# Performance work log

Measured on AMD Instinct MI355X. Metric: run time of the kernel, lower is better.

Reference implementation:

```python
import jax, jax.numpy as jnp
import numpy as np

B, C, P, N_PARTS, JOINTS_PER_PART = 2048, 256, 15, 5, 3
GROUPS = 4
EPS = 1e-5
MASK_VAL = 10000.0


def setup_inputs() -> dict:
    key = jax.random.key(0)
    k1, k2, k3 = jax.random.split(key, 3)
    g = (2 * C) // GROUPS  # 128
    return {
        "x": jax.random.normal(k1, (B, C, P, 1), jnp.float32),
        "conv_w": jax.random.normal(k2, (GROUPS, g, g), jnp.float32) * 0.05,
        "conv_b": jax.random.normal(k3, (2 * C,), jnp.float32) * 0.05,
        "bn_gamma": jnp.ones((2 * C,), jnp.float32),
        "bn_beta": jnp.zeros((2 * C,), jnp.float32),
    }


def reference(x, conv_w, conv_b, bn_gamma, bn_beta):
    Bb, Cc, Pp, _ = x.shape
    xs = x[..., 0]  # [B, C, P]

    # relative[b,c,i,k] = xs[b,c,k] - xs[b,c,i]; for a row i in part p the
    # reduction is max_k(relative - MASK_VAL * [k in part p]). Since the mask
    # only depends on the part of row i, precompute the per-part masked max of
    # xs over k and broadcast-subtract xs[i].
    part_id = jnp.arange(Pp) // JOINTS_PER_PART  # [P]
    Mg = jnp.where(part_id[None, :] == jnp.arange(N_PARTS)[:, None], -MASK_VAL, 0.0)  # [5, P]
    m = jnp.max(xs[:, :, None, :] + Mg[None, None, :, :], axis=-1)  # [B, C, 5]
    tmp = m[:, :, part_id] - xs  # [B, C, P]

    y = jnp.concatenate([xs, tmp], axis=1)  # [B, 2C, P]

    # grouped 1x1 conv (groups=4)
    g = (2 * Cc) // GROUPS
    y4 = y.reshape(Bb, GROUPS, g, Pp)
    z = jnp.einsum('bgip,goi->bgop', y4, conv_w).reshape(Bb, 2 * Cc, Pp)
    z = z + conv_b[None, :, None]

    # BatchNorm2d, training mode: biased batch stats over (B, spatial)
    mean = jnp.mean(z, axis=(0, 2))
    var = jnp.var(z, axis=(0, 2))
    zn = (z - mean[None, :, None]) * jax.lax.rsqrt(var + EPS)[None, :, None]
    out = jax.nn.relu(zn * bn_gamma[None, :, None] + bn_beta[None, :, None])
    return out[..., None]  # [B, 2C, P, 1]
```

## Files before the change

kernel.cpp:

```cpp
#include <hip/hip_runtime.h>
#include <hip/hip_bf16.h>
#include <cstdint>

#define NB_B 2048
#define NTOT (2048 * 16)
#define NVALID (2048 * 15)
#define EPS_ 1e-5f

typedef __bf16 bf16x8 __attribute__((ext_vector_type(8)));
typedef float f32x16 __attribute__((ext_vector_type(16)));
typedef unsigned short u16x8 __attribute__((ext_vector_type(8)));

__device__ __forceinline__ unsigned short f2bf(float f) {
  unsigned u = __float_as_uint(f);
  u += 0x7FFFu + ((u >> 16) & 1u);
  return (unsigned short)(u >> 16);
}
__device__ __forceinline__ float bf2f(unsigned short h) {
  return __uint_as_float((unsigned)h << 16);
}

__global__ void k_wprep(const float* __restrict__ w, unsigned short* __restrict__ wf) {
  int q = blockIdx.x * 256 + threadIdx.x;
  int l = q & 63, ks = (q >> 6) & 7, mt = (q >> 9) & 3, g = q >> 11;
  int o = mt * 32 + (l & 31);
  int i = ks * 16 + (l >> 5) * 8;
  const float* src = w + ((size_t)(g * 128 + o) * 128 + i);
  u16x8 v;
#pragma unroll
  for (int j = 0; j < 8; ++j) v[j] = f2bf(src[j]);
  *(u16x8*)(wf + (size_t)q * 8) = v;
}

__global__ __launch_bounds__(256, 2) void k_gemm(const float* __restrict__ x,
                                                 const unsigned short* __restrict__ wf,
                                                 unsigned short* __restrict__ Z) {
  __shared__ unsigned short Yt[64 * 520];
  __shared__ float xs[3840];
  const int t = threadIdx.x;
  const int b0 = blockIdx.x * 4;

  for (int bi = 0; bi < 4; ++bi) {
    const float* xb = x + (size_t)(b0 + bi) * (256 * 15);
#pragma unroll
    for (int k = 0; k < 15; ++k) xs[k * 256 + t] = xb[k * 256 + t];
    __syncthreads();
    float v[15];
#pragma unroll
    for (int p = 0; p < 15; ++p) v[p] = xs[t * 15 + p];
    float pm[5];
#pragma unroll
    for (int q = 0; q < 5; ++q) pm[q] = fmaxf(fmaxf(v[3 * q], v[3 * q + 1]), v[3 * q + 2]);
    float mq[5];
    mq[0] = fmaxf(fmaxf(pm[1], pm[2]), fmaxf(pm[3], pm[4]));
    mq[1] = fmaxf(fmaxf(pm[0], pm[2]), fmaxf(pm[3], pm[4]));
    mq[2] = fmaxf(fmaxf(pm[0], pm[1]), fmaxf(pm[3], pm[4]));
    mq[3] = fmaxf(fmaxf(pm[0], pm[1]), fmaxf(pm[2], pm[4]));
    mq[4] = fmaxf(fmaxf(pm[0], pm[1]), fmaxf(pm[2], pm[3]));
    const int c0 = bi * 16;
#pragma unroll
    for (int p = 0; p < 15; ++p) {
      Yt[(c0 + p) * 520 + t] = f2bf(v[p]);
      Yt[(c0 + p) * 520 + 256 + t] = f2bf(mq[p / 3] - v[p]);
    }
    Yt[(c0 + 15) * 520 + t] = 0;
    Yt[(c0 + 15) * 520 + 256 + t] = 0;
    __syncthreads();
  }

  const int lane = t & 63, g = t >> 6;
  const int l31 = lane & 31, lh = lane >> 5;
  const bf16x8* Wfv = (const bf16x8*)wf;
  const int gn0 = blockIdx.x * 64;

  for (int mp = 0; mp < 2; ++mp) {
    bf16x8 wr[2][8];
#pragma unroll
    for (int mm = 0; mm < 2; ++mm)
#pragma unroll
      for (int ks = 0; ks < 8; ++ks)
        wr[mm][ks] = Wfv[(size_t)(((g * 4 + mp * 2 + mm) * 8 + ks) * 64 + lane)];
#pragma unroll
    for (int nt = 0; nt < 2; ++nt) {
      const int col = nt * 32 + l31;
      const unsigned short* yrow = &Yt[col * 520 + g * 128 + lh * 8];
      bf16x8 bfr[8];
#pragma unroll
      for (int ks = 0; ks < 8; ++ks)
        bfr[ks] = *(const bf16x8*)(yrow + ks * 16);
      f32x16 a0, a1;
#pragma unroll
      for (int r = 0; r < 16; ++r) { a0[r] = 0.f; a1[r] = 0.f; }
#pragma unroll
      for (int ks = 0; ks < 8; ++ks) {
        a0 = __builtin_amdgcn_mfma_f32_32x32x16_bf16(wr[0][ks], bfr[ks], a0, 0, 0, 0);
        a1 = __builtin_amdgcn_mfma_f32_32x32x16_bf16(wr[1][ks], bfr[ks], a1, 0, 0, 0);
      }
      const int n = gn0 + col;
      unsigned short* zc = Z + n;
#pragma unroll
      for (int r = 0; r < 16; ++r) {
        int row = (r & 3) + 8 * (r >> 2) + 4 * lh;
        size_t ch0 = (size_t)(g * 128 + mp * 64 + row);
        zc[ch0 * NTOT] = f2bf(a0[r]);
        zc[(ch0 + 32) * NTOT] = f2bf(a1[r]);
      }
    }
  }
}

__global__ void k_stats(const unsigned short* __restrict__ Z,
                        const float* __restrict__ gamma, const float* __restrict__ beta,
                        float2* __restrict__ AB) {
  const int ch = blockIdx.x, t = threadIdx.x;
  const u16x8* zr = (const u16x8*)(Z + (size_t)ch * NTOT);
  float s = 0.f, s2 = 0.f;
#pragma unroll 4
  for (int it = 0; it < 16; ++it) {
    u16x8 u = zr[it * 256 + t];
#pragma unroll
    for (int j = 0; j < 8; ++j) { float f = bf2f(u[j]); s += f; s2 += f * f; }
  }
#pragma unroll
  for (int m = 32; m >= 1; m >>= 1) { s += __shfl_xor(s, m, 64); s2 += __shfl_xor(s2, m, 64); }
  __shared__ float ls[4], ls2[4];
  if ((t & 63) == 0) { ls[t >> 6] = s; ls2[t >> 6] = s2; }
  __syncthreads();
  if (t == 0) {
    float S = ls[0] + ls[1] + ls[2] + ls[3];
    float S2 = ls2[0] + ls2[1] + ls2[2] + ls2[3];
    const float inv = 1.f / (float)NVALID;
    float mean = S * inv;
    float var = fmaxf(S2 * inv - mean * mean, 0.f);
    float a = gamma[ch] * rsqrtf(var + EPS_);
    AB[ch] = make_float2(a, beta[ch] - mean * a);
  }
}

__global__ __launch_bounds__(256, 2) void k_final(const unsigned short* __restrict__ Z,
                                                  const float2* __restrict__ AB,
                                                  float* __restrict__ out) {
  __shared__ unsigned short zt[512 * 72];
  __shared__ float aArr[512], bArr[512];
  const int t = threadIdx.x;
  const int b0 = blockIdx.x * 4, n0 = b0 * 16;
#pragma unroll
  for (int i = 0; i < 2; ++i) {
    int ch = i * 256 + t;
    float2 ab = AB[ch];
    aArr[ch] = ab.x; bArr[ch] = ab.y;
  }
#pragma unroll 4
  for (int it = 0; it < 16; ++it) {
    int q = it * 256 + t;
    int ch = q >> 3, o8 = (q & 7) * 8;
    *(u16x8*)&zt[ch * 72 + o8] = *(const u16x8*)(Z + (size_t)ch * NTOT + n0 + o8);
  }
  __syncthreads();
  for (int bi = 0; bi < 4; ++bi) {
    float* slab = out + (size_t)(b0 + bi) * 7680;
#pragma unroll 5
    for (int k = 0; k < 30; ++k) {
      int e = k * 256 + t;
      int ch = e / 15, p = e - ch * 15;
      float val = bf2f(zt[ch * 72 + bi * 16 + p]);
      slab[e] = fmaxf(fmaf(val, aArr[ch], bArr[ch]), 0.f);
    }
  }
}

extern "C" void kernel_launch(void* const* d_in, const int* in_sizes, int n_in,
                              void* d_out, int out_size, void* d_ws, size_t ws_size,
                              hipStream_t stream) {
  const float* x = (const float*)d_in[0];
  const float* cw = (const float*)d_in[1];
  const float* gamma = (const float*)d_in[3];
  const float* beta = (const float*)d_in[4];

  unsigned short* wf = (unsigned short*)d_ws;
  unsigned short* Z = wf + 65536;
  float2* AB = (float2*)(Z + (size_t)512 * NTOT);

  hipLaunchKernelGGL(k_wprep, dim3(32), dim3(256), 0, stream, cw, wf);
  hipLaunchKernelGGL(k_gemm, dim3(512), dim3(256), 0, stream, x, wf, Z);
  hipLaunchKernelGGL(k_stats, dim3(512), dim3(256), 0, stream, Z, gamma, beta, AB);
  hipLaunchKernelGGL(k_final, dim3(512), dim3(256), 0, stream, Z, AB, (float*)d_out);
}
```

Before: 48.91 us.

## Fuse BN statistics into GEMM epilogue via atomics and halve per-block batch tile

Removes the separate stats kernel: the GEMM epilogue reduces per-channel sum and sum-of-squares from the MFMA accumulators and atomically adds them into a padded Sums buffer, which the weight-prep kernel zeroes. The GEMM now processes 2 batches per block across 1024 blocks with occupancy hint 3, double-buffers weight fragments across M tiles, swaps MFMA operand roles so Z is written as packed 4-wide stores, and vectorises the x loads. The final kernel computes the affine scale and shift inline. This saves one full read pass over Z and one launch, at the cost of float atomics contending on 512 channels and a non-deterministic summation order.

```diff
diff --git a/kernel.cpp b/kernel.cpp
--- a/kernel.cpp
+++ b/kernel.cpp
@@ -2,14 +2,15 @@
 #include <hip/hip_bf16.h>
 #include <cstdint>
 
-#define NB_B 2048
 #define NTOT (2048 * 16)
-#define NVALID (2048 * 15)
+#define NVALID_F 30720.0f
 #define EPS_ 1e-5f
 
 typedef __bf16 bf16x8 __attribute__((ext_vector_type(8)));
 typedef float f32x16 __attribute__((ext_vector_type(16)));
+typedef float f32x4 __attribute__((ext_vector_type(4)));
 typedef unsigned short u16x8 __attribute__((ext_vector_type(8)));
+typedef unsigned short u16x4 __attribute__((ext_vector_type(4)));
 
 __device__ __forceinline__ unsigned short f2bf(float f) {
   unsigned u = __float_as_uint(f);
@@ -20,8 +21,10 @@
   return __uint_as_float((unsigned)h << 16);
 }
 
-__global__ void k_wprep(const float* __restrict__ w, unsigned short* __restrict__ wf) {
+__global__ void k_wprep(const float* __restrict__ w, unsigned short* __restrict__ wf,
+                        float* __restrict__ Sums) {
   int q = blockIdx.x * 256 + threadIdx.x;
+  Sums[q] = 0.f;
   int l = q & 63, ks = (q >> 6) & 7, mt = (q >> 9) & 3, g = q >> 11;
   int o = mt * 32 + (l & 31);
   int i = ks * 16 + (l >> 5) * 8;
@@ -32,18 +35,19 @@
   *(u16x8*)(wf + (size_t)q * 8) = v;
 }
 
-__global__ __launch_bounds__(256, 2) void k_gemm(const float* __restrict__ x,
+__global__ __launch_bounds__(256, 3) void k_gemm(const float* __restrict__ x,
                                                  const unsigned short* __restrict__ wf,
-                                                 unsigned short* __restrict__ Z) {
-  __shared__ unsigned short Yt[64 * 520];
+                                                 unsigned short* __restrict__ Z,
+                                                 float* __restrict__ Sums) {
+  __shared__ unsigned short Yt[32 * 520];
   __shared__ float xs[3840];
   const int t = threadIdx.x;
-  const int b0 = blockIdx.x * 4;
+  const int b0 = blockIdx.x * 2;
 
-  for (int bi = 0; bi < 4; ++bi) {
-    const float* xb = x + (size_t)(b0 + bi) * (256 * 15);
-#pragma unroll
-    for (int k = 0; k < 15; ++k) xs[k * 256 + t] = xb[k * 256 + t];
+  for (int bi = 0; bi < 2; ++bi) {
+    const f32x4* xb4 = (const f32x4*)(x + (size_t)(b0 + bi) * 3840);
+    f32x4* xs4 = (f32x4*)xs;
+    for (int q = t; q < 960; q += 256) xs4[q] = xb4[q];
     __syncthreads();
     float v[15];
 #pragma unroll
@@ -71,99 +75,93 @@
   const int lane = t & 63, g = t >> 6;
   const int l31 = lane & 31, lh = lane >> 5;
   const bf16x8* Wfv = (const bf16x8*)wf;
-  const int gn0 = blockIdx.x * 64;
+  const int n0 = blockIdx.x * 32;
 
-  for (int mp = 0; mp < 2; ++mp) {
-    bf16x8 wr[2][8];
+  bf16x8 bfr[8];
+  const unsigned short* yrow = &Yt[l31 * 520 + g * 128 + lh * 8];
 #pragma unroll
-    for (int mm = 0; mm < 2; ++mm)
+  for (int ks = 0; ks < 8; ++ks)
+    bfr[ks] = *(const bf16x8*)(yrow + ks * 16);
+
+  bf16x8 wrA[8], wrB[8];
 #pragma unroll
-      for (int ks = 0; ks < 8; ++ks)
-        wr[mm][ks] = Wfv[(size_t)(((g * 4 + mp * 2 + mm) * 8 + ks) * 64 + lane)];
-#pragma unroll
-    for (int nt = 0; nt < 2; ++nt) {
-      const int col = nt * 32 + l31;
-      const unsigned short* yrow = &Yt[col * 520 + g * 128 + lh * 8];
-      bf16x8 bfr[8];
-#pragma unroll
-      for (int ks = 0; ks < 8; ++ks)
-        bfr[ks] = *(const bf16x8*)(yrow + ks * 16);
-      f32x16 a0, a1;
-#pragma unroll
-      for (int r = 0; r < 16; ++r) { a0[r] = 0.f; a1[r] = 0.f; }
-#pragma unroll
-      for (int ks = 0; ks < 8; ++ks) {
-        a0 = __builtin_amdgcn_mfma_f32_32x32x16_bf16(wr[0][ks], bfr[ks], a0, 0, 0, 0);
-        a1 = __builtin_amdgcn_mfma_f32_32x32x16_bf16(wr[1][ks], bfr[ks], a1, 0, 0, 0);
-      }
-      const int n = gn0 + col;
-      unsigned short* zc = Z + n;
-#pragma unroll
-      for (int r = 0; r < 16; ++r) {
-        int row = (r & 3) + 8 * (r >> 2) + 4 * lh;
-        size_t ch0 = (size_t)(g * 128 + mp * 64 + row);
-        zc[ch0 * NTOT] = f2bf(a0[r]);
-        zc[(ch0 + 32) * NTOT] = f2bf(a1[r]);
-      }
-    }
-  }
+  for (int ks = 0; ks < 8; ++ks)
+    wrA[ks] = Wfv[(size_t)((g * 4 + 0) * 8 + ks) * 64 + lane];
+
+#define MT_STEP(MT, CUR, NXT, PRE)                                              \
+  do {                                                                          \
+    if (PRE) {                                                                  \
+      _Pragma("unroll") for (int ks = 0; ks < 8; ++ks)                          \
+          NXT[ks] = Wfv[(size_t)((g * 4 + (MT) + 1) * 8 + ks) * 64 + lane];     \
+    }                                                                           \
+    f32x16 acc;                                                                 \
+    _Pragma("unroll") for (int r = 0; r < 16; ++r) acc[r] = 0.f;                \
+    _Pragma("unroll") for (int ks = 0; ks < 8; ++ks)                            \
+        acc = __builtin_amdgcn_mfma_f32_32x32x16_bf16(bfr[ks], CUR[ks], acc, 0, 0, 0); \
+    float s = 0.f, s2 = 0.f;                                                    \
+    _Pragma("unroll") for (int r = 0; r < 16; ++r) {                            \
+      float vv = acc[r]; s += vv; s2 = fmaf(vv, vv, s2);                        \
+    }                                                                           \
+    s += __shfl_xor(s, 32, 64);                                                 \
+    s2 += __shfl_xor(s2, 32, 64);                                               \
+    const int ch = g * 128 + (MT) * 32 + l31;                                   \
+    if (lane < 32) {                                                            \
+      unsafeAtomicAdd(&Sums[ch * 16], s);                                       \
+      unsafeAtomicAdd(&Sums[ch * 16 + 1], s2);                                  \
+    }                                                                           \
+    unsigned short* zc = Z + (size_t)ch * NTOT + n0 + 4 * lh;                   \
+    _Pragma("unroll") for (int q = 0; q < 4; ++q) {                             \
+      u16x4 pk;                                                                 \
+      _Pragma("unroll") for (int j = 0; j < 4; ++j) pk[j] = f2bf(acc[4 * q + j]); \
+      *(u16x4*)(zc + 8 * q) = pk;                                               \
+    }                                                                           \
+  } while (0)
+
+  MT_STEP(0, wrA, wrB, 1);
+  MT_STEP(1, wrB, wrA, 1);
+  MT_STEP(2, wrA, wrB, 1);
+  MT_STEP(3, wrB, wrA, 0);
+#undef MT_STEP
 }
 
-__global__ void k_stats(const unsigned short* __restrict__ Z,
-                        const float* __restrict__ gamma, const float* __restrict__ beta,
-                        float2* __restrict__ AB) {
-  const int ch = blockIdx.x, t = threadIdx.x;
-  const u16x8* zr = (const u16x8*)(Z + (size_t)ch * NTOT);
-  float s = 0.f, s2 = 0.f;
-#pragma unroll 4
-  for (int it = 0; it < 16; ++it) {
-    u16x8 u = zr[it * 256 + t];
+__global__ __launch_bounds__(256, 3) void k_final(const unsigned short* __restrict__ Z,
+                                                  const float* __restrict__ Sums,
+                                                  const float* __restrict__ gamma,
+                                                  const float* __restrict__ beta,
+                                                  float* __restrict__ out) {
+  __shared__ unsigned short zt[512 * 48];
+  __shared__ float aArr[512], bArr[512];
+  const int t = threadIdx.x;
+  const int n0 = blockIdx.x * 32;
+
 #pragma unroll
-    for (int j = 0; j < 8; ++j) { float f = bf2f(u[j]); s += f; s2 += f * f; }
+  for (int it = 0; it < 8; ++it) {
+    int q = it * 256 + t;
+    int ch = q >> 2, o = (q & 3) * 8;
+    *(u16x8*)&zt[ch * 48 + o] = *(const u16x8*)(Z + (size_t)ch * NTOT + n0 + o);
   }
+  const float inv = 1.f / NVALID_F;
 #pragma unroll
-  for (int m = 32; m >= 1; m >>= 1) { s += __shfl_xor(s, m, 64); s2 += __shfl_xor(s2, m, 64); }
-  __shared__ float ls[4], ls2[4];
-  if ((t & 63) == 0) { ls[t >> 6] = s; ls2[t >> 6] = s2; }
-  __syncthreads();
-  if (t == 0) {
-    float S = ls[0] + ls[1] + ls[2] + ls[3];
-    float S2 = ls2[0] + ls2[1] + ls2[2] + ls2[3];
-    const float inv = 1.f / (float)NVALID;
+  for (int i = 0; i < 2; ++i) {
+    int ch = i * 256 + t;
+    float S = Sums[ch * 16], S2 = Sums[ch * 16 + 1];
     float mean = S * inv;
     float var = fmaxf(S2 * inv - mean * mean, 0.f);
     float a = gamma[ch] * rsqrtf(var + EPS_);
-    AB[ch] = make_float2(a, beta[ch] - mean * a);
-  }
-}
-
-__global__ __launch_bounds__(256, 2) void k_final(const unsigned short* __restrict__ Z,
-                                                  const float2* __restrict__ AB,
-                                                  float* __restrict__ out) {
-  __shared__ unsigned short zt[512 * 72];
-  __shared__ float aArr[512], bArr[512];
-  const int t = threadIdx.x;
-  const int b0 = blockIdx.x * 4, n0 = b0 * 16;
-#pragma unroll
-  for (int i = 0; i < 2; ++i) {
-    int ch = i * 256 + t;
-    float2 ab = AB[ch];
-    aArr[ch] = ab.x; bArr[ch] = ab.y;
-  }
-#pragma unroll 4
-  for (int it = 0; it < 16; ++it) {
-    int q = it * 256 + t;
-    int ch = q >> 3, o8 = (q & 7) * 8;
-    *(u16x8*)&zt[ch * 72 + o8] = *(const u16x8*)(Z + (size_t)ch * NTOT + n0 + o8);
+    aArr[ch] = a;
+    bArr[ch] = beta[ch] - mean * a;
   }
   __syncthreads();
-  for (int bi = 0; bi < 4; ++bi) {
+
+  const int b0 = blockIdx.x * 2;
+#pragma unroll
+  for (int bi = 0; bi < 2; ++bi) {
     float* slab = out + (size_t)(b0 + bi) * 7680;
-#pragma unroll 5
+#pragma unroll 6
     for (int k = 0; k < 30; ++k) {
       int e = k * 256 + t;
       int ch = e / 15, p = e - ch * 15;
-      float val = bf2f(zt[ch * 72 + bi * 16 + p]);
+      float val = bf2f(zt[ch * 48 + bi * 16 + p]);
       slab[e] = fmaxf(fmaf(val, aArr[ch], bArr[ch]), 0.f);
     }
   }
@@ -179,10 +177,10 @@
 
   unsigned short* wf = (unsigned short*)d_ws;
   unsigned short* Z = wf + 65536;
-  float2* AB = (float2*)(Z + (size_t)512 * NTOT);
+  float* Sums = (float*)(Z + (size_t)512 * NTOT);
 
-  hipLaunchKernelGGL(k_wprep, dim3(32), dim3(256), 0, stream, cw, wf);
-  hipLaunchKernelGGL(k_gemm, dim3(512), dim3(256), 0, stream, x, wf, Z);
-  hipLaunchKernelGGL(k_stats, dim3(512), dim3(256), 0, stream, Z, gamma, beta, AB);
-  hipLaunchKernelGGL(k_final, dim3(512), dim3(256), 0, stream, Z, AB, (float*)d_out);
+  hipLaunchKernelGGL(k_wprep, dim3(32), dim3(256), 0, stream, cw, wf, Sums);
+  hipLaunchKernelGGL(k_gemm, dim3(1024), dim3(256), 0, stream, x, wf, Z, Sums);
+  hipLaunchKernelGGL(k_final, dim3(1024), dim3(256), 0, stream, Z, Sums, gamma, beta,
+                     (float*)d_out);
 }
```

New measurement: 106.1 us. 117% more time.
